# Optimization experiments

Measured on AMD Instinct MI355X. Metric: run time of the kernel, lower is better.

Reference implementation:

```python
import jax, jax.numpy as jnp
import numpy as np

D_MODEL = 1024
N_HEADS = 16
HEAD_DIM = D_MODEL // N_HEADS
B, S = 2, 2048


def setup_inputs() -> dict:
    key = jax.random.key(0)
    ks = jax.random.split(key, 12)
    sd = 1.0 / np.sqrt(D_MODEL)
    inp = {
        "x": jax.random.normal(ks[0], (B, S, D_MODEL), dtype=jnp.float32),
        "rel_bias": jax.random.normal(ks[1], (N_HEADS, S, S), dtype=jnp.float32) * 0.02,
        "attn_mask": jnp.zeros((1, 1, S, S), dtype=jnp.float32),
        # Linear params in torch layout: W [out, in], b [out]
        "Wq": jax.random.normal(ks[2], (D_MODEL, D_MODEL), dtype=jnp.float32) * sd,
        "bq": jnp.zeros((D_MODEL,), dtype=jnp.float32),
        "Wk": jax.random.normal(ks[3], (D_MODEL, D_MODEL), dtype=jnp.float32) * sd,
        "bk": jnp.zeros((D_MODEL,), dtype=jnp.float32),
        "Wv": jax.random.normal(ks[4], (D_MODEL, D_MODEL), dtype=jnp.float32) * sd,
        "bv": jnp.zeros((D_MODEL,), dtype=jnp.float32),
        "Wo": jax.random.normal(ks[5], (D_MODEL, D_MODEL), dtype=jnp.float32) * sd,
        "bo": jnp.zeros((D_MODEL,), dtype=jnp.float32),
    }
    return inp


def _split_heads(t):
    # [B, S, D] -> [B, H, S, Hd]
    b, s, _ = t.shape
    return t.reshape(b, s, N_HEADS, HEAD_DIM).transpose(0, 2, 1, 3)


def reference(x, rel_bias, attn_mask, Wq, bq, Wk, bk, Wv, bv, Wo, bo):
    scale = HEAD_DIM ** (-0.5)
    q = _split_heads(x @ Wq.T + bq)  # [B, H, S, Hd]
    k = _split_heads(x @ Wk.T + bk)
    v = _split_heads(x @ Wv.T + bv)
    scores = jnp.einsum("bhqd,bhkd->bhqk", q, k) * scale
    scores = scores + rel_bias  # [H,S,S] broadcasts over batch
    scores = scores + attn_mask  # [1,1,S,S]
    probs = jax.nn.softmax(scores, axis=-1)
    ctx = jnp.einsum("bhqk,bhkd->bhqd", probs, v)  # [B, H, S, Hd]
    ctx = ctx.transpose(0, 2, 1, 3).reshape(x.shape[0], x.shape[1], D_MODEL)
    return ctx @ Wo.T + bo
```

## Files before the change

### kernel.cpp

```cpp
#include <hip/hip_runtime.h>
#include <hip/hip_bf16.h>
#include <stdint.h>

#define S_LEN 2048
#define DM 1024
#define NH 16
#define HD 64

typedef __bf16 bf16x8 __attribute__((ext_vector_type(8)));
typedef float f32x4 __attribute__((ext_vector_type(4)));
typedef unsigned short u16x4 __attribute__((ext_vector_type(4)));

#if __has_builtin(__builtin_amdgcn_exp2f)
#define EXP2F(x) __builtin_amdgcn_exp2f(x)
#else
#define EXP2F(x) exp2f(x)
#endif

__device__ __forceinline__ unsigned short f2bf(float f){
  union { float f; uint32_t u; } v; v.f = f;
  uint32_t r = v.u + 0x7fffu + ((v.u >> 16) & 1u);
  return (unsigned short)(r >> 16);
}

__device__ __forceinline__ void load_lds16(const void* g, void* l){
  __builtin_amdgcn_global_load_lds((const __attribute__((address_space(1))) void*)g,
                                   (__attribute__((address_space(3))) void*)l, 16, 0, 0);
}

__device__ __forceinline__ f32x4 mfma16(bf16x8 a, bf16x8 b, f32x4 c){
  return __builtin_amdgcn_mfma_f32_16x16x32_bf16(a, b, c, 0, 0, 0);
}

__device__ __forceinline__ bf16x8 lds_swz_read(const unsigned short* base, int row, int cb){
  int addr = (row << 7) + (cb ^ ((row & 7) << 4));
  return *reinterpret_cast<const bf16x8*>(reinterpret_cast<const char*>(base) + addr);
}

__global__ void prep_kernel(const float* __restrict__ x,
                            const float* __restrict__ wq, const float* __restrict__ wk,
                            const float* __restrict__ wv, const float* __restrict__ wo,
                            unsigned short* __restrict__ ws_base){
  long idx = ((long)blockIdx.x * 256 + threadIdx.x) * 4;
  const float* s; unsigned short* d; long off;
  if (idx < (1L << 22)) { s = x; d = ws_base; off = idx; }
  else {
    long r = idx - (1L << 22);
    int wsel = (int)(r >> 20);
    off = r & ((1L << 20) - 1);
    s = wsel == 0 ? wq : wsel == 1 ? wk : wsel == 2 ? wv : wo;
    d = ws_base + (1L << 22) + ((long)wsel << 20);
  }
  float4 f = *reinterpret_cast<const float4*>(s + off);
  u16x4 o;
  o[0] = f2bf(f.x); o[1] = f2bf(f.y); o[2] = f2bf(f.z); o[3] = f2bf(f.w);
  *reinterpret_cast<u16x4*>(d + off) = o;
}

template<int MODE>
__global__ __launch_bounds__(256, 2)
void gemm_bt_kernel(const unsigned short* __restrict__ A,
                    const unsigned short* __restrict__ B0,
                    const unsigned short* __restrict__ B1,
                    const unsigned short* __restrict__ B2,
                    const float* __restrict__ bias0,
                    const float* __restrict__ bias1,
                    const float* __restrict__ bias2,
                    unsigned short* __restrict__ q_out,
                    unsigned short* __restrict__ k_out,
                    unsigned short* __restrict__ vt_out,
                    float* __restrict__ f_out)
{
  __shared__ unsigned short As[128 * 64];
  __shared__ unsigned short Bs[128 * 64];
  const int tid = threadIdx.x;
  const int lane = tid & 63;
  const int w = tid >> 6;
  const int wr = w >> 1, wc = w & 1;
  const int mBase = blockIdx.y * 128;
  int nb = blockIdx.x;
  const unsigned short* Bmat; const float* bias; int mat;
  if constexpr (MODE == 0) {
    mat = nb >> 3;
    nb &= 7;
    Bmat = mat == 0 ? B0 : (mat == 1 ? B1 : B2);
    bias = mat == 0 ? bias0 : (mat == 1 ? bias1 : bias2);
  } else { mat = 0; Bmat = B0; bias = bias0; }
  const int nBase = nb * 128;

  f32x4 acc[4][4] = {};
  const int srow = lane >> 3;
  const int ksrc = ((lane & 7) ^ srow) * 8;
  const unsigned short* ArowBase = A    + (size_t)(mBase + w * 32 + srow) * DM + ksrc;
  const unsigned short* BrowBase = Bmat + (size_t)(nBase + w * 32 + srow) * DM + ksrc;

  for (int kt = 0; kt < 16; ++kt) {
    #pragma unroll
    for (int i = 0; i < 4; ++i) {
      load_lds16(ArowBase + (size_t)(i * 8) * DM + kt * 64, &As[(w * 4 + i) * 512]);
      load_lds16(BrowBase + (size_t)(i * 8) * DM + kt * 64, &Bs[(w * 4 + i) * 512]);
    }
    __syncthreads();
    #pragma unroll
    for (int kk = 0; kk < 2; ++kk) {
      bf16x8 af[4], bfr[4];
      const int cb = kk * 64 + ((lane >> 4) << 4);
      #pragma unroll
      for (int m = 0; m < 4; ++m)
        af[m] = lds_swz_read(As, wr * 64 + m * 16 + (lane & 15), cb);
      #pragma unroll
      for (int n = 0; n < 4; ++n)
        bfr[n] = lds_swz_read(Bs, wc * 64 + n * 16 + (lane & 15), cb);
      #pragma unroll
      for (int m = 0; m < 4; ++m)
        #pragma unroll
        for (int n = 0; n < 4; ++n)
          acc[m][n] = mfma16(af[m], bfr[n], acc[m][n]);
    }
    __syncthreads();
  }

  #pragma unroll
  for (int m = 0; m < 4; ++m) {
    #pragma unroll
    for (int n = 0; n < 4; ++n) {
      const int col = nBase + wc * 64 + n * 16 + (lane & 15);
      const float bv = bias[col];
      const int row0 = mBase + wr * 64 + m * 16 + ((lane >> 4) << 2);
      if constexpr (MODE == 1) {
        #pragma unroll
        for (int j = 0; j < 4; ++j)
          f_out[(size_t)(row0 + j) * DM + col] = acc[m][n][j] + bv;
      } else {
        const int h = col >> 6, d = col & 63;
        if (mat < 2) {
          unsigned short* dst = (mat == 0) ? q_out : k_out;
          #pragma unroll
          for (int j = 0; j < 4; ++j) {
            const int row = row0 + j;
            const int b = row >> 11, s = row & 2047;
            dst[(((size_t)b * NH + h) * S_LEN + s) * HD + d] = f2bf(acc[m][n][j] + bv);
          }
        } else {
          const int b = row0 >> 11, s = row0 & 2047;
          u16x4 pk;
          #pragma unroll
          for (int j = 0; j < 4; ++j) pk[j] = f2bf(acc[m][n][j] + bv);
          *reinterpret_cast<u16x4*>(&vt_out[(((size_t)b * NH + h) * HD + d) * S_LEN + s]) = pk;
        }
      }
    }
  }
}


#define LOAD_RAW(kvB) do {                                                    \
    rb0 = *reinterpret_cast<const f32x4*>(bp + (kvB) + g * 4);                \
    rm0 = *reinterpret_cast<const f32x4*>(mp + (kvB) + g * 4);                \
    rb1 = *reinterpret_cast<const f32x4*>(bp + (kvB) + 16 + g * 4);           \
    rm1 = *reinterpret_cast<const f32x4*>(mp + (kvB) + 16 + g * 4);           \
    rb2 = *reinterpret_cast<const f32x4*>(bp + (kvB) + 32 + g * 4);           \
    rm2 = *reinterpret_cast<const f32x4*>(mp + (kvB) + 32 + g * 4);           \
    rb3 = *reinterpret_cast<const f32x4*>(bp + (kvB) + 48 + g * 4);           \
    rm3 = *reinterpret_cast<const f32x4*>(mp + (kvB) + 48 + g * 4);           \
  } while (0)

#define COMBINE do {                                                          \
    bm0 = (rb0 + rm0) * L2E; bm1 = (rb1 + rm1) * L2E;                         \
    bm2 = (rb2 + rm2) * L2E; bm3 = (rb3 + rm3) * L2E;                         \
  } while (0)

#define STAGE(kvB, buf) do {                                                                \
    load_lds16(Kp + (size_t)((kvB) + w * 16 + srow) * HD + ksrc,      &Ks[buf][(w * 2) * 512]);     \
    load_lds16(Vp + (size_t)(w * 16 + srow) * S_LEN + (kvB) + ksrc,   &Vs[buf][(w * 2) * 512]);     \
    load_lds16(Kp + (size_t)((kvB) + w * 16 + 8 + srow) * HD + ksrc,  &Ks[buf][(w * 2 + 1) * 512]); \
    load_lds16(Vp + (size_t)(w * 16 + 8 + srow) * S_LEN + (kvB) + ksrc, &Vs[buf][(w * 2 + 1) * 512]); \
  } while (0)

#define QK_COL(NN, SCN) do {                                                  \
    bf16x8 kf0_ = lds_swz_read(KSB_, (NN) * 16 + q, cbq);                     \
    bf16x8 kf1_ = lds_swz_read(KSB_, (NN) * 16 + q, 64 + cbq);                \
    f32x4 z_ = {};                                                            \
    z_ = mfma16(kf0_, qf0, z_);                                               \
    SCN = mfma16(kf1_, qf1, z_);                                              \
  } while (0)

#define BIAS_COL(SCN, BMN) do {                                               \
    SCN[0] = SCN[0] * SC + BMN[0];                                            \
    SCN[1] = SCN[1] * SC + BMN[1];                                            \
    SCN[2] = SCN[2] * SC + BMN[2];                                            \
    SCN[3] = SCN[3] * SC + BMN[3];                                            \
    mt_ = fmaxf(mt_, fmaxf(fmaxf(SCN[0], SCN[1]), fmaxf(SCN[2], SCN[3])));    \
  } while (0)

#define EXP_COL(SCN) do {                                                     \
    SCN[0] = EXP2F(SCN[0] - mn_); SCN[1] = EXP2F(SCN[1] - mn_);               \
    SCN[2] = EXP2F(SCN[2] - mn_); SCN[3] = EXP2F(SCN[3] - mn_);               \
  } while (0)

#define PWR_COL(NN, SCN) do {                                                 \
    u16x4 pk_;                                                                \
    pk_[0] = f2bf(SCN[0]); pk_[1] = f2bf(SCN[1]);                             \
    pk_[2] = f2bf(SCN[2]); pk_[3] = f2bf(SCN[3]);                             \
    const int colb_ = ((NN) * 16 + 4 * g) * 2;                                \
    *reinterpret_cast<u16x4*>(                                                \
        reinterpret_cast<char*>(Pw_) + (q << 7) + (colb_ ^ ((q & 7) << 4))) = pk_; \
  } while (0)

#define PV_COL(NN, ACCN) do {                                                 \
    bf16x8 vf0_ = lds_swz_read(VSB_, (NN) * 16 + q, cbq);                     \
    bf16x8 vf1_ = lds_swz_read(VSB_, (NN) * 16 + q, 64 + cbq);                \
    ACCN = mfma16(vf0_, pf0_, ACCN);                                          \
    ACCN = mfma16(vf1_, pf1_, ACCN);                                          \
  } while (0)

#define COMPUTE_TILE(KSB, VSB) do {                                           \
    const unsigned short* KSB_ = (KSB);                                       \
    const unsigned short* VSB_ = (VSB);                                       \
    f32x4 sc0_, sc1_, sc2_, sc3_;                                             \
    QK_COL(0, sc0_); QK_COL(1, sc1_); QK_COL(2, sc2_); QK_COL(3, sc3_);       \
    float mt_ = -3.0e38f;                                                     \
    BIAS_COL(sc0_, bm0); BIAS_COL(sc1_, bm1);                                 \
    BIAS_COL(sc2_, bm2); BIAS_COL(sc3_, bm3);                                 \
    mt_ = fmaxf(mt_, __shfl_xor(mt_, 16));                                    \
    mt_ = fmaxf(mt_, __shfl_xor(mt_, 32));                                    \
    const float mn_ = fmaxf(m_run, mt_);                                      \
    const float corr_ = EXP2F(m_run - mn_);                                   \
    m_run = mn_;                                                              \
    EXP_COL(sc0_); EXP_COL(sc1_); EXP_COL(sc2_); EXP_COL(sc3_);               \
    f32x4 ls4_ = sc0_ + sc1_ + sc2_ + sc3_;                                   \
    float ls_ = ls4_[0] + ls4_[1] + ls4_[2] + ls4_[3];                        \
    ls_ += __shfl_xor(ls_, 16);                                               \
    ls_ += __shfl_xor(ls_, 32);                                               \
    l_run = l_run * corr_ + ls_;                                              \
    acc0_ *= corr_; acc1_ *= corr_; acc2_ *= corr_; acc3_ *= corr_;           \
    unsigned short* Pw_ = Ps[w];                                              \
    PWR_COL(0, sc0_); PWR_COL(1, sc1_); PWR_COL(2, sc2_); PWR_COL(3, sc3_);   \
    bf16x8 pf0_ = lds_swz_read(Pw_, q, cbq);                                  \
    bf16x8 pf1_ = lds_swz_read(Pw_, q, 64 + cbq);                             \
    PV_COL(0, acc0_); PV_COL(1, acc1_); PV_COL(2, acc2_); PV_COL(3, acc3_);   \
  } while (0)

__global__ __launch_bounds__(256) __attribute__((amdgpu_waves_per_eu(3, 4)))
void attn_kernel(const unsigned short* __restrict__ Q,
                 const unsigned short* __restrict__ Kmat,
                 const unsigned short* __restrict__ Vt,
                 const float* __restrict__ rel_bias,
                 const float* __restrict__ mask,
                 unsigned short* __restrict__ ctx)
{
  __shared__ unsigned short Ks[2][64 * 64];
  __shared__ unsigned short Vs[2][64 * 64];
  __shared__ unsigned short Ps[4][16 * 64];

  const int logical = (blockIdx.x & 7) * 128 + (blockIdx.x >> 3);
  const int b  = logical & 1;
  const int qt = (logical >> 1) & 31;
  const int h  = logical >> 6;

  const int lane = threadIdx.x & 63, w = threadIdx.x >> 6;
  const int q = lane & 15, g = lane >> 4;
  const size_t bh = (size_t)b * NH + h;
  const int qRow = qt * 64 + w * 16;
  const unsigned short* Qp = Q + (bh * S_LEN + qRow) * HD;
  bf16x8 qf0 = *reinterpret_cast<const bf16x8*>(Qp + (size_t)q * HD + g * 8);
  bf16x8 qf1 = *reinterpret_cast<const bf16x8*>(Qp + (size_t)q * HD + 32 + g * 8);

  const unsigned short* Kp = Kmat + bh * (size_t)S_LEN * HD;
  const unsigned short* Vp = Vt + bh * (size_t)HD * S_LEN;
  const float* bp = rel_bias + (size_t)h * S_LEN * S_LEN + (size_t)(qRow + q) * S_LEN;
  const float* mp = mask + (size_t)(qRow + q) * S_LEN;

  float m_run = -3.0e38f, l_run = 0.f;
  f32x4 acc0_ = {}, acc1_ = {}, acc2_ = {}, acc3_ = {};
  f32x4 rb0, rb1, rb2, rb3, rm0, rm1, rm2, rm3;
  f32x4 bm0, bm1, bm2, bm3;

  const float SC  = 0.125f * 1.44269504089f;
  const float L2E = 1.44269504089f;

  const int srow = lane >> 3;
  const int ksrc = ((lane & 7) ^ srow) * 8;
  const int cbq = g << 4;

  LOAD_RAW(0);
  STAGE(0, 0);
  __syncthreads();

  for (int i = 0; i < 16; ++i) {
    const int t0 = 2 * i;
    COMBINE;
    LOAD_RAW((t0 + 1) * 64);
    STAGE((t0 + 1) * 64, 1);
    COMPUTE_TILE(Ks[0], Vs[0]);
    __syncthreads();
    COMBINE;
    if (i < 15) {
      LOAD_RAW((t0 + 2) * 64);
      STAGE((t0 + 2) * 64, 0);
    }
    COMPUTE_TILE(Ks[1], Vs[1]);
    __syncthreads();
  }

  const float inv = 1.0f / l_run;
  acc0_ *= inv; acc1_ *= inv; acc2_ *= inv; acc3_ *= inv;
  unsigned short* Pw_ = Ps[w];
  PWR_COL(0, acc0_); PWR_COL(1, acc1_); PWR_COL(2, acc2_); PWR_COL(3, acc3_);
  bf16x8 c0 = lds_swz_read(Pw_, q, g << 4);
  bf16x8 c1 = lds_swz_read(Pw_, q, 64 + (g << 4));
  unsigned short* cp = ctx + ((size_t)b * S_LEN + qRow + q) * DM + h * HD;
  *reinterpret_cast<bf16x8*>(cp + 8 * g) = c0;
  *reinterpret_cast<bf16x8*>(cp + 32 + 8 * g) = c1;
}

extern "C" void kernel_launch(void* const* d_in, const int* in_sizes, int n_in,
                              void* d_out, int out_size, void* d_ws, size_t ws_size,
                              hipStream_t stream) {
  (void)in_sizes; (void)n_in; (void)out_size; (void)ws_size;
  const float* x  = (const float*)d_in[0];
  const float* rb = (const float*)d_in[1];
  const float* mk = (const float*)d_in[2];
  const float* Wq = (const float*)d_in[3];
  const float* bq = (const float*)d_in[4];
  const float* Wk = (const float*)d_in[5];
  const float* bk = (const float*)d_in[6];
  const float* Wv = (const float*)d_in[7];
  const float* bv = (const float*)d_in[8];
  const float* Wo = (const float*)d_in[9];
  const float* bo = (const float*)d_in[10];
  float* out = (float*)d_out;

  unsigned short* ws  = (unsigned short*)d_ws;
  unsigned short* xb  = ws;
  unsigned short* wqb = ws + (1L << 22);
  unsigned short* wkb = wqb + (1L << 20);
  unsigned short* wvb = wkb + (1L << 20);
  unsigned short* wob = wvb + (1L << 20);
  unsigned short* Qw  = wob + (1L << 20);
  unsigned short* Kw  = Qw + (1L << 22);
  unsigned short* Vtw = Kw + (1L << 22);
  unsigned short* ctx = Vtw + (1L << 22);

  prep_kernel<<<8192, 256, 0, stream>>>(x, Wq, Wk, Wv, Wo, ws);
  gemm_bt_kernel<0><<<dim3(24, 32), 256, 0, stream>>>(
      xb, wqb, wkb, wvb, bq, bk, bv, Qw, Kw, Vtw, nullptr);
  attn_kernel<<<1024, 256, 0, stream>>>(Qw, Kw, Vtw, rb, mk, ctx);
  gemm_bt_kernel<1><<<dim3(8, 32), 256, 0, stream>>>(
      ctx, wob, nullptr, nullptr, bo, nullptr, nullptr, nullptr, nullptr, nullptr, out);
}
```

Measured before the change: 237.6 us.

## Split attention KV range in two with merge kernel and single-buffered LDS

The attention kernel now splits each query tile's KV range into two halves, which doubles the grid to 2048 blocks. It writes partial contexts plus the running max and sum to workspace, and a new merge kernel combines the two halves. LDS is cut to a single K/V buffer with explicit vmcnt waits and sched barriers, and the occupancy hint is raised to 5-8 waves per EU. The goal is more parallelism and occupancy on the memory-bound bias stream. The cost is an extra kernel launch, extra partial-context traffic, and less overlap of loads with compute within a block.

```diff
diff --git a/kernel.cpp b/kernel.cpp
--- a/kernel.cpp
+++ b/kernel.cpp
@@ -21,6 +21,11 @@
   union { float f; uint32_t u; } v; v.f = f;
   uint32_t r = v.u + 0x7fffu + ((v.u >> 16) & 1u);
   return (unsigned short)(r >> 16);
+}
+
+__device__ __forceinline__ float bf2f(unsigned short u){
+  union { uint32_t u; float f; } v; v.u = ((uint32_t)u) << 16;
+  return v.f;
 }
 
 __device__ __forceinline__ void load_lds16(const void* g, void* l){
@@ -154,15 +159,21 @@
 }
 
 
-#define LOAD_RAW(kvB) do {                                                    \
-    rb0 = *reinterpret_cast<const f32x4*>(bp + (kvB) + g * 4);                \
-    rm0 = *reinterpret_cast<const f32x4*>(mp + (kvB) + g * 4);                \
-    rb1 = *reinterpret_cast<const f32x4*>(bp + (kvB) + 16 + g * 4);           \
-    rm1 = *reinterpret_cast<const f32x4*>(mp + (kvB) + 16 + g * 4);           \
-    rb2 = *reinterpret_cast<const f32x4*>(bp + (kvB) + 32 + g * 4);           \
-    rm2 = *reinterpret_cast<const f32x4*>(mp + (kvB) + 32 + g * 4);           \
-    rb3 = *reinterpret_cast<const f32x4*>(bp + (kvB) + 48 + g * 4);           \
-    rm3 = *reinterpret_cast<const f32x4*>(mp + (kvB) + 48 + g * 4);           \
+#define WAITV8 do { asm volatile("s_waitcnt vmcnt(8)" ::: "memory"); } while (0)
+#define WAITV4 do { asm volatile("s_waitcnt vmcnt(4)" ::: "memory"); } while (0)
+#define WAITV0 do { asm volatile("s_waitcnt vmcnt(0)" ::: "memory"); } while (0)
+#define SB0    __builtin_amdgcn_sched_barrier(0)
+#define BAR    __builtin_amdgcn_s_barrier()
+
+#define LOAD_RAW(lB) do {                                                     \
+    rb0 = *reinterpret_cast<const f32x4*>(bp + (lB) + g * 4);                 \
+    rm0 = *reinterpret_cast<const f32x4*>(mp + (lB) + g * 4);                 \
+    rb1 = *reinterpret_cast<const f32x4*>(bp + (lB) + 16 + g * 4);            \
+    rm1 = *reinterpret_cast<const f32x4*>(mp + (lB) + 16 + g * 4);            \
+    rb2 = *reinterpret_cast<const f32x4*>(bp + (lB) + 32 + g * 4);            \
+    rm2 = *reinterpret_cast<const f32x4*>(mp + (lB) + 32 + g * 4);            \
+    rb3 = *reinterpret_cast<const f32x4*>(bp + (lB) + 48 + g * 4);            \
+    rm3 = *reinterpret_cast<const f32x4*>(mp + (lB) + 48 + g * 4);            \
   } while (0)
 
 #define COMBINE do {                                                          \
@@ -170,19 +181,14 @@
     bm2 = (rb2 + rm2) * L2E; bm3 = (rb3 + rm3) * L2E;                         \
   } while (0)
 
-#define STAGE(kvB, buf) do {                                                                \
-    load_lds16(Kp + (size_t)((kvB) + w * 16 + srow) * HD + ksrc,      &Ks[buf][(w * 2) * 512]);     \
-    load_lds16(Vp + (size_t)(w * 16 + srow) * S_LEN + (kvB) + ksrc,   &Vs[buf][(w * 2) * 512]);     \
-    load_lds16(Kp + (size_t)((kvB) + w * 16 + 8 + srow) * HD + ksrc,  &Ks[buf][(w * 2 + 1) * 512]); \
-    load_lds16(Vp + (size_t)(w * 16 + 8 + srow) * S_LEN + (kvB) + ksrc, &Vs[buf][(w * 2 + 1) * 512]); \
-  } while (0)
-
-#define QK_COL(NN, SCN) do {                                                  \
-    bf16x8 kf0_ = lds_swz_read(KSB_, (NN) * 16 + q, cbq);                     \
-    bf16x8 kf1_ = lds_swz_read(KSB_, (NN) * 16 + q, 64 + cbq);                \
-    f32x4 z_ = {};                                                            \
-    z_ = mfma16(kf0_, qf0, z_);                                               \
-    SCN = mfma16(kf1_, qf1, z_);                                              \
+#define STAGE_K(kvB) do {                                                                    \
+    load_lds16(Kp + (size_t)((kvB) + w * 16 + srow) * HD + ksrc,     &Ks[(w * 2) * 512]);    \
+    load_lds16(Kp + (size_t)((kvB) + w * 16 + 8 + srow) * HD + ksrc, &Ks[(w * 2 + 1) * 512]);\
+  } while (0)
+
+#define STAGE_V(kvB) do {                                                                    \
+    load_lds16(Vp + (size_t)(w * 16 + srow) * S_LEN + (kvB) + ksrc,     &Vs[(w * 2) * 512]);    \
+    load_lds16(Vp + (size_t)(w * 16 + 8 + srow) * S_LEN + (kvB) + ksrc, &Vs[(w * 2 + 1) * 512]);\
   } while (0)
 
 #define BIAS_COL(SCN, BMN) do {                                               \
@@ -207,18 +213,20 @@
         reinterpret_cast<char*>(Pw_) + (q << 7) + (colb_ ^ ((q & 7) << 4))) = pk_; \
   } while (0)
 
-#define PV_COL(NN, ACCN) do {                                                 \
-    bf16x8 vf0_ = lds_swz_read(VSB_, (NN) * 16 + q, cbq);                     \
-    bf16x8 vf1_ = lds_swz_read(VSB_, (NN) * 16 + q, 64 + cbq);                \
-    ACCN = mfma16(vf0_, pf0_, ACCN);                                          \
-    ACCN = mfma16(vf1_, pf1_, ACCN);                                          \
-  } while (0)
-
-#define COMPUTE_TILE(KSB, VSB) do {                                           \
-    const unsigned short* KSB_ = (KSB);                                       \
-    const unsigned short* VSB_ = (VSB);                                       \
+#define COMPUTE_TILE do {                                                     \
     f32x4 sc0_, sc1_, sc2_, sc3_;                                             \
-    QK_COL(0, sc0_); QK_COL(1, sc1_); QK_COL(2, sc2_); QK_COL(3, sc3_);       \
+    { bf16x8 a_ = lds_swz_read(Ks, 0 * 16 + q, cbq);                          \
+      bf16x8 b_ = lds_swz_read(Ks, 0 * 16 + q, 64 + cbq);                     \
+      f32x4 z_ = {}; z_ = mfma16(a_, qf0, z_); sc0_ = mfma16(b_, qf1, z_); }  \
+    { bf16x8 a_ = lds_swz_read(Ks, 1 * 16 + q, cbq);                          \
+      bf16x8 b_ = lds_swz_read(Ks, 1 * 16 + q, 64 + cbq);                     \
+      f32x4 z_ = {}; z_ = mfma16(a_, qf0, z_); sc1_ = mfma16(b_, qf1, z_); }  \
+    { bf16x8 a_ = lds_swz_read(Ks, 2 * 16 + q, cbq);                          \
+      bf16x8 b_ = lds_swz_read(Ks, 2 * 16 + q, 64 + cbq);                     \
+      f32x4 z_ = {}; z_ = mfma16(a_, qf0, z_); sc2_ = mfma16(b_, qf1, z_); }  \
+    { bf16x8 a_ = lds_swz_read(Ks, 3 * 16 + q, cbq);                          \
+      bf16x8 b_ = lds_swz_read(Ks, 3 * 16 + q, 64 + cbq);                     \
+      f32x4 z_ = {}; z_ = mfma16(a_, qf0, z_); sc3_ = mfma16(b_, qf1, z_); }  \
     float mt_ = -3.0e38f;                                                     \
     BIAS_COL(sc0_, bm0); BIAS_COL(sc1_, bm1);                                 \
     BIAS_COL(sc2_, bm2); BIAS_COL(sc3_, bm3);                                 \
@@ -234,42 +242,57 @@
     ls_ += __shfl_xor(ls_, 32);                                               \
     l_run = l_run * corr_ + ls_;                                              \
     acc0_ *= corr_; acc1_ *= corr_; acc2_ *= corr_; acc3_ *= corr_;           \
-    unsigned short* Pw_ = Ps[w];                                              \
     PWR_COL(0, sc0_); PWR_COL(1, sc1_); PWR_COL(2, sc2_); PWR_COL(3, sc3_);   \
     bf16x8 pf0_ = lds_swz_read(Pw_, q, cbq);                                  \
     bf16x8 pf1_ = lds_swz_read(Pw_, q, 64 + cbq);                             \
-    PV_COL(0, acc0_); PV_COL(1, acc1_); PV_COL(2, acc2_); PV_COL(3, acc3_);   \
-  } while (0)
-
-__global__ __launch_bounds__(256) __attribute__((amdgpu_waves_per_eu(3, 4)))
+    { bf16x8 a_ = lds_swz_read(Vs, 0 * 16 + q, cbq);                          \
+      bf16x8 b_ = lds_swz_read(Vs, 0 * 16 + q, 64 + cbq);                     \
+      acc0_ = mfma16(a_, pf0_, acc0_); acc0_ = mfma16(b_, pf1_, acc0_); }     \
+    { bf16x8 a_ = lds_swz_read(Vs, 1 * 16 + q, cbq);                          \
+      bf16x8 b_ = lds_swz_read(Vs, 1 * 16 + q, 64 + cbq);                     \
+      acc1_ = mfma16(a_, pf0_, acc1_); acc1_ = mfma16(b_, pf1_, acc1_); }     \
+    { bf16x8 a_ = lds_swz_read(Vs, 2 * 16 + q, cbq);                          \
+      bf16x8 b_ = lds_swz_read(Vs, 2 * 16 + q, 64 + cbq);                     \
+      acc2_ = mfma16(a_, pf0_, acc2_); acc2_ = mfma16(b_, pf1_, acc2_); }     \
+    { bf16x8 a_ = lds_swz_read(Vs, 3 * 16 + q, cbq);                          \
+      bf16x8 b_ = lds_swz_read(Vs, 3 * 16 + q, 64 + cbq);                     \
+      acc3_ = mfma16(a_, pf0_, acc3_); acc3_ = mfma16(b_, pf1_, acc3_); }     \
+  } while (0)
+
+__global__ __launch_bounds__(256) __attribute__((amdgpu_waves_per_eu(5, 8)))
 void attn_kernel(const unsigned short* __restrict__ Q,
                  const unsigned short* __restrict__ Kmat,
                  const unsigned short* __restrict__ Vt,
                  const float* __restrict__ rel_bias,
                  const float* __restrict__ mask,
-                 unsigned short* __restrict__ ctx)
+                 unsigned short* __restrict__ ctxp0,
+                 unsigned short* __restrict__ ctxp1,
+                 float* __restrict__ Mbuf,
+                 float* __restrict__ Lbuf)
 {
-  __shared__ unsigned short Ks[2][64 * 64];
-  __shared__ unsigned short Vs[2][64 * 64];
+  __shared__ unsigned short Ks[64 * 64];
+  __shared__ unsigned short Vs[64 * 64];
   __shared__ unsigned short Ps[4][16 * 64];
 
-  const int logical = (blockIdx.x & 7) * 128 + (blockIdx.x >> 3);
-  const int b  = logical & 1;
-  const int qt = (logical >> 1) & 31;
-  const int h  = logical >> 6;
+  const int logical = (blockIdx.x & 7) * 256 + (blockIdx.x >> 3);
+  const int s  = logical & 1;
+  const int b  = (logical >> 1) & 1;
+  const int qt = (logical >> 2) & 31;
+  const int h  = logical >> 7;
 
   const int lane = threadIdx.x & 63, w = threadIdx.x >> 6;
   const int q = lane & 15, g = lane >> 4;
-  const size_t bh = (size_t)b * NH + h;
+  const int bh = b * NH + h;
   const int qRow = qt * 64 + w * 16;
-  const unsigned short* Qp = Q + (bh * S_LEN + qRow) * HD;
+  const int kv0 = s << 10;
+  const unsigned short* Qp = Q + ((size_t)bh * S_LEN + qRow) * HD;
   bf16x8 qf0 = *reinterpret_cast<const bf16x8*>(Qp + (size_t)q * HD + g * 8);
   bf16x8 qf1 = *reinterpret_cast<const bf16x8*>(Qp + (size_t)q * HD + 32 + g * 8);
 
-  const unsigned short* Kp = Kmat + bh * (size_t)S_LEN * HD;
-  const unsigned short* Vp = Vt + bh * (size_t)HD * S_LEN;
-  const float* bp = rel_bias + (size_t)h * S_LEN * S_LEN + (size_t)(qRow + q) * S_LEN;
-  const float* mp = mask + (size_t)(qRow + q) * S_LEN;
+  const unsigned short* Kp = Kmat + (size_t)bh * S_LEN * HD;
+  const unsigned short* Vp = Vt + (size_t)bh * HD * S_LEN;
+  const float* bp = rel_bias + (size_t)h * S_LEN * S_LEN + (size_t)(qRow + q) * S_LEN + kv0;
+  const float* mp = mask + (size_t)(qRow + q) * S_LEN + kv0;
 
   float m_run = -3.0e38f, l_run = 0.f;
   f32x4 acc0_ = {}, acc1_ = {}, acc2_ = {}, acc3_ = {};
@@ -282,36 +305,76 @@
   const int srow = lane >> 3;
   const int ksrc = ((lane & 7) ^ srow) * 8;
   const int cbq = g << 4;
+  unsigned short* Pw_ = Ps[w];
 
   LOAD_RAW(0);
-  STAGE(0, 0);
-  __syncthreads();
-
-  for (int i = 0; i < 16; ++i) {
-    const int t0 = 2 * i;
+  SB0;
+
+  for (int t = 0; t < 15; ++t) {
+    const int kvB = kv0 + t * 64;
+    BAR;
+    STAGE_K(kvB); STAGE_V(kvB);
+    SB0;
+    WAITV4; SB0;
     COMBINE;
-    LOAD_RAW((t0 + 1) * 64);
-    STAGE((t0 + 1) * 64, 1);
-    COMPUTE_TILE(Ks[0], Vs[0]);
-    __syncthreads();
+    LOAD_RAW((t + 1) * 64);
+    SB0;
+    WAITV8; SB0;
+    BAR;
+    COMPUTE_TILE;
+  }
+  {
+    const int kvB = kv0 + 15 * 64;
+    BAR;
+    STAGE_K(kvB); STAGE_V(kvB);
+    SB0;
+    WAITV4; SB0;
     COMBINE;
-    if (i < 15) {
-      LOAD_RAW((t0 + 2) * 64);
-      STAGE((t0 + 2) * 64, 0);
-    }
-    COMPUTE_TILE(Ks[1], Vs[1]);
-    __syncthreads();
+    WAITV0; SB0;
+    BAR;
+    COMPUTE_TILE;
   }
 
   const float inv = 1.0f / l_run;
   acc0_ *= inv; acc1_ *= inv; acc2_ *= inv; acc3_ *= inv;
-  unsigned short* Pw_ = Ps[w];
   PWR_COL(0, acc0_); PWR_COL(1, acc1_); PWR_COL(2, acc2_); PWR_COL(3, acc3_);
   bf16x8 c0 = lds_swz_read(Pw_, q, g << 4);
   bf16x8 c1 = lds_swz_read(Pw_, q, 64 + (g << 4));
-  unsigned short* cp = ctx + ((size_t)b * S_LEN + qRow + q) * DM + h * HD;
+  unsigned short* cp = (s ? ctxp1 : ctxp0) +
+                       ((size_t)(b * S_LEN + qRow + q)) * DM + h * HD;
   *reinterpret_cast<bf16x8*>(cp + 8 * g) = c0;
   *reinterpret_cast<bf16x8*>(cp + 32 + 8 * g) = c1;
+  if (g == 0) {
+    const int mlIdx = (s << 16) + (bh << 11) + qRow + q;
+    Mbuf[mlIdx] = m_run;
+    Lbuf[mlIdx] = l_run;
+  }
+}
+
+__global__ void merge_kernel(const unsigned short* __restrict__ ctxp0,
+                             const unsigned short* __restrict__ ctxp1,
+                             const float* __restrict__ Mbuf,
+                             const float* __restrict__ Lbuf,
+                             unsigned short* __restrict__ ctx){
+  const long e = ((long)blockIdx.x * 256 + threadIdx.x) * 4;
+  const int b = (int)(e >> 21);
+  const int srow = (int)((e >> 10) & 2047);
+  const int d = (int)(e & 1023);
+  const int h = d >> 6;
+  const int idx = ((b * NH + h) << 11) + srow;
+  const float m0 = Mbuf[idx],  m1 = Mbuf[(1 << 16) + idx];
+  const float l0 = Lbuf[idx],  l1 = Lbuf[(1 << 16) + idx];
+  const float mm = fmaxf(m0, m1);
+  const float w0 = EXP2F(m0 - mm) * l0;
+  const float w1 = EXP2F(m1 - mm) * l1;
+  const float inv = 1.0f / (w0 + w1);
+  u16x4 c0 = *reinterpret_cast<const u16x4*>(ctxp0 + e);
+  u16x4 c1 = *reinterpret_cast<const u16x4*>(ctxp1 + e);
+  u16x4 o;
+  #pragma unroll
+  for (int j = 0; j < 4; ++j)
+    o[j] = f2bf((bf2f(c0[j]) * w0 + bf2f(c1[j]) * w1) * inv);
+  *reinterpret_cast<u16x4*>(ctx + e) = o;
 }
 
 extern "C" void kernel_launch(void* const* d_in, const int* in_sizes, int n_in,
@@ -341,11 +404,15 @@
   unsigned short* Kw  = Qw + (1L << 22);
   unsigned short* Vtw = Kw + (1L << 22);
   unsigned short* ctx = Vtw + (1L << 22);
+  unsigned short* ctxp1 = xb;
+  float* Mb = (float*)wqb;
+  float* Lb = (float*)(wqb + (1L << 19));
 
   prep_kernel<<<8192, 256, 0, stream>>>(x, Wq, Wk, Wv, Wo, ws);
   gemm_bt_kernel<0><<<dim3(24, 32), 256, 0, stream>>>(
       xb, wqb, wkb, wvb, bq, bk, bv, Qw, Kw, Vtw, nullptr);
-  attn_kernel<<<1024, 256, 0, stream>>>(Qw, Kw, Vtw, rb, mk, ctx);
+  attn_kernel<<<2048, 256, 0, stream>>>(Qw, Kw, Vtw, rb, mk, ctx, ctxp1, Mb, Lb);
+  merge_kernel<<<4096, 256, 0, stream>>>(ctx, ctxp1, Mb, Lb, ctx);
   gemm_bt_kernel<1><<<dim3(8, 32), 256, 0, stream>>>(
       ctx, wob, nullptr, nullptr, bo, nullptr, nullptr, nullptr, nullptr, nullptr, out);
 }
```

Result: slower. 410.1 us (+72.6%).
